# Optimization experiments

Hardware: AMD Instinct MI355X
Metric: run time of the kernel (lower is better)

## Reference

```python
import jax, jax.numpy as jnp
import numpy as np

NH = 32      # num_attention_heads
HD = 128     # head dim (kv_channels)
NG = 2       # multi_query_group_num
LAYER_NUMBER = 1


def apply_rotary_pos_emb(x, rope_cache):
    # x: [b, np, sq, hn]; rope_cache: [1, sq_max, rot/2, 2]
    b, nh, sq, hn = x.shape
    rot_dim = rope_cache.shape[-2] * 2
    xr, x_pass = x[..., :rot_dim], x[..., rot_dim:]
    xs = xr.reshape(b, nh, sq, rot_dim // 2, 2)
    c = rope_cache[:, :sq].reshape(-1, 1, sq, rot_dim // 2, 2)
    out = jnp.stack(
        [xs[..., 0] * c[..., 0] - xs[..., 1] * c[..., 1],
         xs[..., 1] * c[..., 0] + xs[..., 0] * c[..., 1]], axis=-1)
    out = out.reshape(b, nh, sq, rot_dim)
    return jnp.concatenate([out, x_pass], axis=-1)


def setup_inputs() -> dict:
    key = jax.random.key(0)
    ks = jax.random.split(key, 5)
    b, sq, h = 2, 2048, 4096
    qkv_out = NH * HD + 2 * NG * HD  # 4608
    return {
        "hidden_states": jax.random.normal(ks[0], (b, sq, h), jnp.float32),
        "rope_cache": jax.random.normal(ks[1], (1, sq, HD // 4, 2), jnp.float32),
        "W_qkv": jax.random.normal(ks[2], (h, qkv_out), jnp.float32) * 0.02,
        "b_qkv": jax.random.normal(ks[3], (qkv_out,), jnp.float32) * 0.02,
        "W_dense": jax.random.normal(ks[4], (NH * HD, h), jnp.float32) * 0.02,
    }


def reference(hidden_states, rope_cache, W_qkv, b_qkv, W_dense):
    b, sq, h = hidden_states.shape
    mixed = hidden_states @ W_qkv + b_qkv  # [b, sq, nh*hd + 2*ng*hd]
    q_sz = NH * HD
    kv_sz = NG * HD
    q = mixed[..., :q_sz].reshape(b, sq, NH, HD).transpose(0, 2, 1, 3)          # [b,nh,sq,hd]
    k = mixed[..., q_sz:q_sz + kv_sz].reshape(b, sq, NG, HD).transpose(0, 2, 1, 3)  # [b,ng,sq,hd]
    v = mixed[..., q_sz + kv_sz:].reshape(b, sq, NG, HD).transpose(0, 2, 1, 3)      # [b,ng,sq,hd]

    q = apply_rotary_pos_emb(q, rope_cache)
    k = apply_rotary_pos_emb(k, rope_cache)

    # expand KV groups to full heads (multi-query attention)
    rep = NH // NG
    k = jnp.broadcast_to(k[:, :, None], (b, NG, rep, sq, HD)).reshape(b, NH, sq, HD)
    v = jnp.broadcast_to(v[:, :, None], (b, NG, rep, sq, HD)).reshape(b, NH, sq, HD)

    # CoreAttention (eager path, fp32 softmax, causal)
    coeff = float(max(1, LAYER_NUMBER))  # apply_query_key_layer_scaling
    norm_factor = np.sqrt(HD) * coeff
    scores = jnp.einsum("bhqd,bhkd->bhqk", q, k) / norm_factor
    scores = scores.astype(jnp.float32) * coeff
    causal = jnp.tril(jnp.ones((sq, sq), dtype=bool))
    scores = jnp.where(causal[None, None], scores, -jnp.inf)
    probs = jax.nn.softmax(scores, axis=-1).astype(v.dtype)
    context = jnp.einsum("bhqk,bhkd->bhqd", probs, v)   # [b,nh,sq,hd]
    context = context.transpose(0, 2, 1, 3).reshape(b, sq, NH * HD)
    return context @ W_dense
```

## Files before the change

### kernel.cpp

```cpp
#include <hip/hip_runtime.h>
#include <hip/hip_bf16.h>
#include <stdint.h>

#define B_    2
#define SQ    2048
#define H_    4096
#define NHEAD 32
#define HDIM  128
#define NGRP  2
#define QKVN  4608
#define SCALE 0.08838834764831845f
#define QSCALE (0.08838834764831845f * 1.4426950408889634f)

typedef __attribute__((ext_vector_type(8))) short bf16x8;
typedef __attribute__((ext_vector_type(4))) short bf16x4;
typedef __attribute__((ext_vector_type(4))) float f32x4;

__device__ __forceinline__ float b2f(short s) {
  union { float f; unsigned u; } x; x.u = ((unsigned)(unsigned short)s) << 16; return x.f;
}
__device__ __forceinline__ short f2b(float f) {
  union { float f; unsigned u; } x; x.f = f;
  unsigned r = x.u + 0x7fffu + ((x.u >> 16) & 1u);
  return (short)(r >> 16);
}
__device__ __forceinline__ void gll16(const void* g, void* l) {
  __builtin_amdgcn_global_load_lds(
      (const __attribute__((address_space(1))) unsigned int*)g,
      (__attribute__((address_space(3))) unsigned int*)l, 16, 0, 0);
}

__global__ void conv_f32_bf16(const float* __restrict__ x, short* __restrict__ y, int n) {
  int i = (blockIdx.x * blockDim.x + threadIdx.x) * 4;
  if (i >= n) return;
  float4 v = *(const float4*)(x + i);
  union { short s[4]; uint2 u; } o;
  o.s[0] = f2b(v.x); o.s[1] = f2b(v.y); o.s[2] = f2b(v.z); o.s[3] = f2b(v.w);
  *(uint2*)(y + i) = o.u;
}

__global__ void transpose_f32_bf16(const float* __restrict__ W, short* __restrict__ Wt,
                                   int R, int C) {
  __shared__ float tile[64][65];
  int c0 = blockIdx.x * 64, r0 = blockIdx.y * 64;
  int tx = threadIdx.x & 15, ty = threadIdx.x >> 4;
  #pragma unroll
  for (int i = 0; i < 4; ++i) {
    float4 v = *(const float4*)(W + (size_t)(r0 + ty + 16 * i) * C + c0 + tx * 4);
    tile[ty + 16 * i][tx * 4 + 0] = v.x;
    tile[ty + 16 * i][tx * 4 + 1] = v.y;
    tile[ty + 16 * i][tx * 4 + 2] = v.z;
    tile[ty + 16 * i][tx * 4 + 3] = v.w;
  }
  __syncthreads();
  #pragma unroll
  for (int i = 0; i < 4; ++i) {
    int orow = ty + 16 * i;
    bf16x4 o;
    #pragma unroll
    for (int j = 0; j < 4; ++j) o[j] = f2b(tile[tx * 4 + j][orow]);
    *(bf16x4*)(Wt + (size_t)(c0 + orow) * R + r0 + tx * 4) = o;
  }
}

template<bool BIAS, bool OUTF32>
__global__ __launch_bounds__(256, 2) void gemm_bf16(
    const short* __restrict__ A, const short* __restrict__ Bt,
    const float* __restrict__ bias, short* __restrict__ outb,
    float* __restrict__ outf, int M, int N, int K)
{
  __shared__ short smA[128 * 64];
  __shared__ short smB[128 * 64];
  const int t = threadIdx.x;
  const int l = t & 63;
  const int w = t >> 6;
  const int wr = w >> 1, wc = w & 1;
  const int m0 = blockIdx.y * 128, n0 = blockIdx.x * 128;

  const f32x4 z = {0.f, 0.f, 0.f, 0.f};
  f32x4 acc[4][4];
  #pragma unroll
  for (int m = 0; m < 4; ++m)
    #pragma unroll
    for (int n = 0; n < 4; ++n) acc[m][n] = z;

  for (int k0 = 0; k0 < K; k0 += 64) {
    __syncthreads();
    #pragma unroll
    for (int i = 0; i < 4; ++i) {
      int c = t + i * 256;
      int row = c >> 3, slot = c & 7;
      int ss = slot ^ (row & 7);
      gll16(A  + (size_t)(m0 + row) * K + k0 + ss * 8,
            (char*)smA + (i * 256 + w * 64) * 16);
      gll16(Bt + (size_t)(n0 + row) * K + k0 + ss * 8,
            (char*)smB + (i * 256 + w * 64) * 16);
    }
    __syncthreads();
    #pragma unroll
    for (int kk = 0; kk < 2; ++kk) {
      bf16x8 a[4], b[4];
      #pragma unroll
      for (int m = 0; m < 4; ++m) {
        int row = wr * 64 + m * 16 + (l & 15);
        int off = (kk * 64 + ((l >> 4) << 4)) ^ ((row & 7) << 4);
        a[m] = *(const bf16x8*)((const char*)smA + row * 128 + off);
      }
      #pragma unroll
      for (int n = 0; n < 4; ++n) {
        int row = wc * 64 + n * 16 + (l & 15);
        int off = (kk * 64 + ((l >> 4) << 4)) ^ ((row & 7) << 4);
        b[n] = *(const bf16x8*)((const char*)smB + row * 128 + off);
      }
      #pragma unroll
      for (int m = 0; m < 4; ++m)
        #pragma unroll
        for (int n = 0; n < 4; ++n)
          acc[m][n] = __builtin_amdgcn_mfma_f32_16x16x32_bf16(a[m], b[n], acc[m][n], 0, 0, 0);
    }
  }

  #pragma unroll
  for (int m = 0; m < 4; ++m) {
    int row = m0 + wr * 64 + m * 16 + ((l >> 4) << 2);
    #pragma unroll
    for (int n = 0; n < 4; ++n) {
      int col = n0 + wc * 64 + n * 16 + (l & 15);
      float bv = BIAS ? bias[col] : 0.f;
      #pragma unroll
      for (int j = 0; j < 4; ++j) {
        float vv = acc[m][n][j] + bv;
        if (OUTF32) outf[(size_t)(row + j) * N + col] = vv;
        else        outb[(size_t)(row + j) * N + col] = f2b(vv);
      }
    }
  }
}

__global__ void rope_split(const short* __restrict__ mixed, const float* __restrict__ rope,
                           short* __restrict__ qo, short* __restrict__ ko, short* __restrict__ vo)
{
  const int CH = QKVN / 8;
  int idx = blockIdx.x * blockDim.x + threadIdx.x;
  if (idx >= B_ * SQ * CH) return;
  int row = idx / CH;
  int cc = (idx - row * CH) * 8;
  int b = row >> 11, s = row & 2047;

  bf16x8 xv = *(const bf16x8*)(mixed + (size_t)row * QKVN + cc);
  float x[8];
  #pragma unroll
  for (int i = 0; i < 8; ++i) x[i] = b2f(xv[i]);

  int sect, hh, d = cc & 127;
  if (cc < 4096)      { sect = 0; hh = cc >> 7; }
  else if (cc < 4352) { sect = 1; hh = (cc - 4096) >> 7; }
  else                { sect = 2; hh = (cc - 4352) >> 7; }

  if (sect < 2 && d < 64) {
    float4 ca = *(const float4*)(rope + s * 64 + d);
    float4 cb = *(const float4*)(rope + s * 64 + d + 4);
    float t0;
    t0 = x[0]*ca.x - x[1]*ca.y; x[1] = x[1]*ca.x + x[0]*ca.y; x[0] = t0;
    t0 = x[2]*ca.z - x[3]*ca.w; x[3] = x[3]*ca.z + x[2]*ca.w; x[2] = t0;
    t0 = x[4]*cb.x - x[5]*cb.y; x[5] = x[5]*cb.x + x[4]*cb.y; x[4] = t0;
    t0 = x[6]*cb.z - x[7]*cb.w; x[7] = x[7]*cb.z + x[6]*cb.w; x[6] = t0;
  }
  if (sect == 0) {
    #pragma unroll
    for (int i = 0; i < 8; ++i) x[i] *= QSCALE;
  }

  short* dst; size_t oidx;
  if (sect == 0)      { dst = qo; oidx = (((size_t)(b * NHEAD + hh) * SQ) + s) * HDIM + d; }
  else if (sect == 1) { dst = ko; oidx = (((size_t)(b * NGRP + hh) * SQ) + s) * HDIM + d; }
  else                { dst = vo; oidx = (((size_t)(b * NGRP + hh) * SQ) + s) * HDIM + d; }
  bf16x8 ov;
  #pragma unroll
  for (int i = 0; i < 8; ++i) ov[i] = f2b(x[i]);
  *(bf16x8*)(dst + oidx) = ov;
}

__global__ __launch_bounds__(512, 2) void attn_fwd(
    const short* __restrict__ q, const short* __restrict__ k,
    const short* __restrict__ v, short* __restrict__ ctx)
{
  __shared__ short smem[8192 + 9216];
  short* smK = smem;
  short* smV = smem + 8192;

  const int h = blockIdx.y, b = blockIdx.z;
  const int g = h >> 4;
  const int t = threadIdx.x, l = t & 63, w = t >> 6;
  const int lq = l & 15, hi = l >> 4;

  const short* qbase = q + ((size_t)(b * NHEAD + h) * SQ) * HDIM;
  const short* kbase = k + ((size_t)(b * NGRP + g) * SQ) * HDIM;
  const short* vbase = v + ((size_t)(b * NGRP + g) * SQ) * HDIM;

  const f32x4 z = {0.f, 0.f, 0.f, 0.f};

  for (int pass = 0; pass < 2; ++pass) {
    const int s = pass ? (7 - (int)blockIdx.x) : (int)blockIdx.x;
    const int q0 = s * 256;
    const int qw = q0 + w * 32;
    const int nkt = 4 * s + 4;

    bf16x8 qf[2][4];
    #pragma unroll
    for (int fq = 0; fq < 2; ++fq)
      #pragma unroll
      for (int kf = 0; kf < 4; ++kf)
        qf[fq][kf] = *(const bf16x8*)(qbase + (size_t)(qw + fq * 16 + lq) * HDIM + kf * 32 + hi * 8);

    f32x4 of[2][8];
    #pragma unroll
    for (int a = 0; a < 2; ++a)
      #pragma unroll
      for (int d = 0; d < 8; ++d) of[a][d] = z;
    float mrow[2] = {-1e30f, -1e30f};
    float lrow[2] = {0.f, 0.f};

    for (int kt = 0; kt < nkt; ++kt) {
      const int kb = kt * 64;
      __syncthreads();
      #pragma unroll
      for (int i = 0; i < 2; ++i) {
        int c = t + i * 512;
        int row = c >> 4, slot = c & 15;
        int ss = slot ^ (row & 7);
        gll16(kbase + (size_t)(kb + row) * HDIM + ss * 8,
              (char*)smK + (i * 512 + w * 64) * 16);
      }
      #pragma unroll
      for (int i = 0; i < 2; ++i) {
        int c = t + i * 512;
        int key = c & 63, d0 = (c >> 6) << 3;
        bf16x8 vv = *(const bf16x8*)(vbase + (size_t)(kb + key) * HDIM + d0);
        #pragma unroll
        for (int jj = 0; jj < 8; ++jj)
          smV[(d0 + jj) * 72 + key] = vv[jj];
      }
      __syncthreads();

      if (kb > qw + 31) continue;

      f32x4 st[2][4];
      #pragma unroll
      for (int fq = 0; fq < 2; ++fq)
        #pragma unroll
        for (int fk = 0; fk < 4; ++fk) st[fq][fk] = z;
      __builtin_amdgcn_s_setprio(1);
      #pragma unroll
      for (int kf = 0; kf < 4; ++kf) {
        bf16x8 kfr[4];
        #pragma unroll
        for (int fk = 0; fk < 4; ++fk) {
          int row = fk * 16 + lq;
          int slot = (kf * 4 + hi) ^ (row & 7);
          kfr[fk] = *(const bf16x8*)((const char*)smK + row * 256 + slot * 16);
        }
        #pragma unroll
        for (int fq = 0; fq < 2; ++fq)
          #pragma unroll
          for (int fk = 0; fk < 4; ++fk)
            st[fq][fk] = __builtin_amdgcn_mfma_f32_16x16x32_bf16(kfr[fk], qf[fq][kf], st[fq][fk], 0, 0, 0);
      }
      __builtin_amdgcn_s_setprio(0);

      bf16x4 pa[2][4];
      #pragma unroll
      for (int fq = 0; fq < 2; ++fq) {
        float sv[16];
        #pragma unroll
        for (int fk = 0; fk < 4; ++fk)
          #pragma unroll
          for (int j = 0; j < 4; ++j) sv[fk * 4 + j] = st[fq][fk][j];
        if (kb + 63 > qw + fq * 16) {
          int qrow = qw + fq * 16 + lq;
          #pragma unroll
          for (int fk = 0; fk < 4; ++fk)
            #pragma unroll
            for (int j = 0; j < 4; ++j)
              if (kb + fk * 16 + hi * 4 + j > qrow) sv[fk * 4 + j] = -1e30f;
        }
        float mx = sv[0];
        #pragma unroll
        for (int i = 1; i < 16; ++i) mx = fmaxf(mx, sv[i]);
        mx = fmaxf(mx, __shfl_xor(mx, 16));
        mx = fmaxf(mx, __shfl_xor(mx, 32));
        if (__any(mx > mrow[fq] + 11.0f)) {
          float mn = fmaxf(mrow[fq], mx);
          float corr = exp2f(mrow[fq] - mn);
          mrow[fq] = mn;
          lrow[fq] *= corr;
          float cj[4];
          #pragma unroll
          for (int j = 0; j < 4; ++j) cj[j] = __shfl(corr, hi * 4 + j);
          #pragma unroll
          for (int df = 0; df < 8; ++df)
            #pragma unroll
            for (int j = 0; j < 4; ++j) of[fq][df][j] *= cj[j];
        }
        float rs = 0.f;
        #pragma unroll
        for (int i = 0; i < 16; ++i) { sv[i] = exp2f(sv[i] - mrow[fq]); rs += sv[i]; }
        rs += __shfl_xor(rs, 16);
        rs += __shfl_xor(rs, 32);
        lrow[fq] += rs;
        #pragma unroll
        for (int fk = 0; fk < 4; ++fk) {
          bf16x4 p;
          p[0] = f2b(sv[fk * 4 + 0]); p[1] = f2b(sv[fk * 4 + 1]);
          p[2] = f2b(sv[fk * 4 + 2]); p[3] = f2b(sv[fk * 4 + 3]);
          pa[fq][fk] = p;
        }
      }

      __builtin_amdgcn_s_setprio(1);
      #pragma unroll
      for (int fk = 0; fk < 4; ++fk) {
        bf16x4 vb[8];
        #pragma unroll
        for (int df = 0; df < 8; ++df)
          vb[df] = *(const bf16x4*)(smV + (df * 16 + lq) * 72 + fk * 16 + hi * 4);
        #pragma unroll
        for (int df = 0; df < 8; ++df) {
          of[0][df] = __builtin_amdgcn_mfma_f32_16x16x16bf16_1k(pa[0][fk], vb[df], of[0][df], 0, 0, 0);
          of[1][df] = __builtin_amdgcn_mfma_f32_16x16x16bf16_1k(pa[1][fk], vb[df], of[1][df], 0, 0, 0);
        }
      }
      __builtin_amdgcn_s_setprio(0);
    }

    #pragma unroll
    for (int fq = 0; fq < 2; ++fq) {
      float inv = 1.f / lrow[fq];
      float ij[4];
      #pragma unroll
      for (int j = 0; j < 4; ++j) ij[j] = __shfl(inv, hi * 4 + j);
      #pragma unroll
      for (int j = 0; j < 4; ++j) {
        int srow = qw + fq * 16 + hi * 4 + j;
        size_t rbase = ((size_t)(b * SQ + srow)) * (NHEAD * HDIM) + (size_t)h * HDIM;
        #pragma unroll
        for (int df = 0; df < 8; ++df)
          ctx[rbase + df * 16 + lq] = f2b(of[fq][df][j] * ij[j]);
      }
    }
    __syncthreads();
  }
}

extern "C" void kernel_launch(void* const* d_in, const int* in_sizes, int n_in,
                              void* d_out, int out_size, void* d_ws, size_t ws_size,
                              hipStream_t stream)
{
  const float* hidden = (const float*)d_in[0];
  const float* rope   = (const float*)d_in[1];
  const float* Wqkv   = (const float*)d_in[2];
  const float* bqkv   = (const float*)d_in[3];
  const float* Wd     = (const float*)d_in[4];
  float* out = (float*)d_out;

  if (ws_size < 113246208ULL) return;
  char* ws = (char*)d_ws;
  short* hsb   = (short*)(ws);
  short* wT    = (short*)(ws + 33554432);
  short* mixed = (short*)(ws + 71303168);
  short* k_r   = (short*)(ws + 109051904);
  short* v_r   = (short*)(ws + 111149056);

  conv_f32_bf16<<<16384, 256, 0, stream>>>(hidden, hsb, B_ * SQ * H_);
  transpose_f32_bf16<<<dim3(QKVN / 64, H_ / 64), 256, 0, stream>>>(Wqkv, wT, H_, QKVN);
  gemm_bf16<true, false><<<dim3(QKVN / 128, (B_ * SQ) / 128), 256, 0, stream>>>(
      hsb, wT, bqkv, mixed, nullptr, B_ * SQ, QKVN, H_);
  rope_split<<<9216, 256, 0, stream>>>(mixed, rope, hsb, k_r, v_r);
  transpose_f32_bf16<<<dim3(H_ / 64, H_ / 64), 256, 0, stream>>>(Wd, wT, H_, H_);
  attn_fwd<<<dim3(4, NHEAD, B_), 512, 0, stream>>>(hsb, k_r, v_r, mixed);
  gemm_bf16<false, true><<<dim3(H_ / 128, (B_ * SQ) / 128), 256, 0, stream>>>(
      mixed, wT, nullptr, nullptr, out, B_ * SQ, H_, H_);
}
```

Measured before the change: 538.6 us.

## Replace dense output GEMM with 256x256-tile, 8-wave phased pipelined kernel

Swaps the final context@W_dense GEMM from the generic 128x128 bf16 kernel to a new kernel with 256x256 tiles, 512 threads and 128KB of double-buffered shared memory. Direct global-to-LDS loads use an XOR swizzle and are spread across four compute phases per K step. MFMA sections run at raised wave priority to overlap loads with math. The larger tile cuts global traffic per FLOP, but the grid shrinks to 256 blocks and the kernel uses heavy LDS and registers, which limits occupancy.

```diff
diff --git a/kernel.cpp b/kernel.cpp
--- a/kernel.cpp
+++ b/kernel.cpp
@@ -133,6 +133,110 @@
         if (OUTF32) outf[(size_t)(row + j) * N + col] = vv;
         else        outb[(size_t)(row + j) * N + col] = f2b(vv);
       }
+    }
+  }
+}
+
+__global__ __launch_bounds__(512, 2) void gemm8ph(
+    const short* __restrict__ A, const short* __restrict__ Bt,
+    float* __restrict__ outf, int M, int N, int K, int nbx)
+{
+  __shared__ char sm[131072];
+  const int t = threadIdx.x, l = t & 63, w = t >> 6;
+  const int lq = l & 15, hi = l >> 4;
+  const int wm = w >> 2, wn = w & 3;
+  const int by = (int)blockIdx.x / nbx, bx = (int)blockIdx.x % nbx;
+  const int m0 = by * 256, n0 = bx * 256;
+  const int nkt = K >> 6;
+
+  auto stage = [&](int tt, int s) {
+    if (tt >= nkt) return;
+    int kb = tt << 6;
+    const short* base = (s < 2) ? Bt + (size_t)(n0 + (s << 7)) * K
+                                : A  + (size_t)(m0 + ((s - 2) << 7)) * K;
+    char* dst = sm + ((tt & 1) << 16) + (s < 2 ? 32768 + (s << 14) : ((s - 2) << 14));
+    #pragma unroll
+    for (int i = 0; i < 2; ++i) {
+      int c = (i << 9) + t;
+      int row = c >> 3, sl = c & 7;
+      gll16(base + (size_t)row * K + kb + ((sl ^ (row & 7)) << 3), dst + c * 16);
+    }
+  };
+
+  const f32x4 z = {0.f, 0.f, 0.f, 0.f};
+  f32x4 acc[8][4];
+  #pragma unroll
+  for (int i = 0; i < 8; ++i)
+    #pragma unroll
+    for (int j = 0; j < 4; ++j) acc[i][j] = z;
+
+  bf16x8 aC[2][2], bC[4][2];
+
+  stage(0, 0); stage(0, 1); stage(0, 2); stage(0, 3);
+  stage(1, 0); stage(1, 1); stage(1, 2);
+  asm volatile("s_waitcnt vmcnt(6)" ::: "memory");
+  __builtin_amdgcn_s_barrier();
+
+#define PH(P, STT, STS, TAILV)                                              \
+  {                                                                         \
+    if ((P) == 0) {                                                         \
+      _Pragma("unroll")                                                     \
+      for (int fn = 0; fn < 4; ++fn) {                                      \
+        int rb = (wn << 6) + (fn << 4) + lq;                                \
+        const char* bb = sm + (bsel << 16) + 32768 + ((rb >> 7) << 14)      \
+                         + (rb & 127) * 128;                                \
+        _Pragma("unroll")                                                   \
+        for (int kk = 0; kk < 2; ++kk)                                      \
+          bC[fn][kk] = *(const bf16x8*)(bb + ((((kk << 2) + hi) ^ (rb & 7)) << 4)); \
+      }                                                                     \
+    }                                                                       \
+    _Pragma("unroll")                                                       \
+    for (int fr = 0; fr < 2; ++fr) {                                        \
+      int lr = ((P) << 5) + (fr << 4) + lq;                                 \
+      const char* ab = sm + (bsel << 16) + (wm << 14) + lr * 128;           \
+      _Pragma("unroll")                                                     \
+      for (int kk = 0; kk < 2; ++kk)                                        \
+        aC[fr][kk] = *(const bf16x8*)(ab + ((((kk << 2) + hi) ^ (lr & 7)) << 4)); \
+    }                                                                       \
+    stage((STT), (STS));                                                    \
+    __builtin_amdgcn_s_barrier();                                           \
+    asm volatile("s_waitcnt lgkmcnt(0)" ::: "memory");                      \
+    __builtin_amdgcn_s_setprio(1);                                          \
+    _Pragma("unroll")                                                       \
+    for (int kk = 0; kk < 2; ++kk)                                          \
+      _Pragma("unroll")                                                     \
+      for (int fr = 0; fr < 2; ++fr)                                        \
+        _Pragma("unroll")                                                   \
+        for (int fn = 0; fn < 4; ++fn)                                      \
+          acc[(P) * 2 + fr][fn] = __builtin_amdgcn_mfma_f32_16x16x32_bf16(  \
+              aC[fr][kk], bC[fn][kk], acc[(P) * 2 + fr][fn], 0, 0, 0);      \
+    __builtin_amdgcn_s_setprio(0);                                          \
+    if ((P) == 3) {                                                         \
+      if (TAILV) asm volatile("s_waitcnt vmcnt(0)" ::: "memory");           \
+      else       asm volatile("s_waitcnt vmcnt(6)" ::: "memory");           \
+    }                                                                       \
+    __builtin_amdgcn_s_barrier();                                           \
+  }
+
+  for (int T = 0; T < nkt; ++T) {
+    const int bsel = T & 1;
+    const bool tail = (T >= nkt - 2);
+    PH(0, T + 1, 3, tail)
+    PH(1, T + 2, 0, tail)
+    PH(2, T + 2, 1, tail)
+    PH(3, T + 2, 2, tail)
+  }
+#undef PH
+
+  #pragma unroll
+  for (int fm = 0; fm < 8; ++fm) {
+    int r0 = m0 + (wm << 7) + (fm << 4) + (hi << 2);
+    #pragma unroll
+    for (int fn = 0; fn < 4; ++fn) {
+      int cc = n0 + (wn << 6) + (fn << 4) + lq;
+      #pragma unroll
+      for (int j = 0; j < 4; ++j)
+        outf[(size_t)(r0 + j) * N + cc] = acc[fm][fn][j];
     }
   }
 }
@@ -378,6 +482,5 @@
   rope_split<<<9216, 256, 0, stream>>>(mixed, rope, hsb, k_r, v_r);
   transpose_f32_bf16<<<dim3(H_ / 64, H_ / 64), 256, 0, stream>>>(Wd, wT, H_, H_);
   attn_fwd<<<dim3(4, NHEAD, B_), 512, 0, stream>>>(hsb, k_r, v_r, mixed);
-  gemm_bf16<false, true><<<dim3(H_ / 128, (B_ * SQ) / 128), 256, 0, stream>>>(
-      mixed, wT, nullptr, nullptr, out, B_ * SQ, H_, H_);
-}
+  gemm8ph<<<256, 512, 0, stream>>>(mixed, wT, out, B_ * SQ, H_, H_, H_ / 256);
+}
```

Result: slower. 552.4 us (+2.6%).

## Double-buffer K/V tiles in attention kernel to overlap loads with compute

Applied to the files above, without the earlier changes.

Splits the shared-memory K and V tiles into two buffers and issues the global loads for the next key tile before computing the current one. The V transpose store into LDS is deferred until after the MFMA work, and there is now one barrier per iteration instead of two. This is meant to hide global-memory latency behind the QK and PV matrix math. In exchange, LDS use doubles (about 69KB per block), which may limit the two-blocks-per-CU occupancy, and the prefetched V values stay live in registers across the compute.

```diff
diff --git a/kernel.cpp b/kernel.cpp
--- a/kernel.cpp
+++ b/kernel.cpp
@@ -185,9 +185,7 @@
     const short* __restrict__ q, const short* __restrict__ k,
     const short* __restrict__ v, short* __restrict__ ctx)
 {
-  __shared__ short smem[8192 + 9216];
-  short* smK = smem;
-  short* smV = smem + 8192;
+  __shared__ short smem[2 * (8192 + 9216)];
 
   const int h = blockIdx.y, b = blockIdx.z;
   const int g = h >> 4;
@@ -197,6 +195,12 @@
   const short* qbase = q + ((size_t)(b * NHEAD + h) * SQ) * HDIM;
   const short* kbase = k + ((size_t)(b * NGRP + g) * SQ) * HDIM;
   const short* vbase = v + ((size_t)(b * NGRP + g) * SQ) * HDIM;
+
+  const int kc0 = t, kc1 = t + 512;
+  const int krow0 = kc0 >> 4, kss0 = (kc0 & 15) ^ (krow0 & 7);
+  const int krow1 = kc1 >> 4, kss1 = (kc1 & 15) ^ (krow1 & 7);
+  const int vkey0 = kc0 & 63, vd0 = (kc0 >> 6) << 3;
+  const int vkey1 = kc1 & 63, vd1 = (kc1 >> 6) << 3;
 
   const f32x4 z = {0.f, 0.f, 0.f, 0.f};
 
@@ -221,116 +225,135 @@
     float mrow[2] = {-1e30f, -1e30f};
     float lrow[2] = {0.f, 0.f};
 
+    {
+      short* K0 = smem;
+      short* V0 = smem + 16384;
+      gll16(kbase + (size_t)krow0 * HDIM + kss0 * 8, (char*)K0 + kc0 * 16);
+      gll16(kbase + (size_t)krow1 * HDIM + kss1 * 8, (char*)K0 + kc1 * 16);
+      bf16x8 vv0 = *(const bf16x8*)(vbase + (size_t)vkey0 * HDIM + vd0);
+      bf16x8 vv1 = *(const bf16x8*)(vbase + (size_t)vkey1 * HDIM + vd1);
+      #pragma unroll
+      for (int jj = 0; jj < 8; ++jj) V0[(vd0 + jj) * 72 + vkey0] = vv0[jj];
+      #pragma unroll
+      for (int jj = 0; jj < 8; ++jj) V0[(vd1 + jj) * 72 + vkey1] = vv1[jj];
+    }
+    __syncthreads();
+
     for (int kt = 0; kt < nkt; ++kt) {
       const int kb = kt * 64;
-      __syncthreads();
-      #pragma unroll
-      for (int i = 0; i < 2; ++i) {
-        int c = t + i * 512;
-        int row = c >> 4, slot = c & 15;
-        int ss = slot ^ (row & 7);
-        gll16(kbase + (size_t)(kb + row) * HDIM + ss * 8,
-              (char*)smK + (i * 512 + w * 64) * 16);
-      }
-      #pragma unroll
-      for (int i = 0; i < 2; ++i) {
-        int c = t + i * 512;
-        int key = c & 63, d0 = (c >> 6) << 3;
-        bf16x8 vv = *(const bf16x8*)(vbase + (size_t)(kb + key) * HDIM + d0);
-        #pragma unroll
-        for (int jj = 0; jj < 8; ++jj)
-          smV[(d0 + jj) * 72 + key] = vv[jj];
-      }
-      __syncthreads();
-
-      if (kb > qw + 31) continue;
-
-      f32x4 st[2][4];
-      #pragma unroll
-      for (int fq = 0; fq < 2; ++fq)
-        #pragma unroll
-        for (int fk = 0; fk < 4; ++fk) st[fq][fk] = z;
-      __builtin_amdgcn_s_setprio(1);
-      #pragma unroll
-      for (int kf = 0; kf < 4; ++kf) {
-        bf16x8 kfr[4];
-        #pragma unroll
-        for (int fk = 0; fk < 4; ++fk) {
-          int row = fk * 16 + lq;
-          int slot = (kf * 4 + hi) ^ (row & 7);
-          kfr[fk] = *(const bf16x8*)((const char*)smK + row * 256 + slot * 16);
+      const int cur = kt & 1;
+      const short* Kc = smem + cur * 8192;
+      const short* Vc = smem + 16384 + cur * 9216;
+      short* Kn = smem + (cur ^ 1) * 8192;
+      short* Vn = smem + 16384 + (cur ^ 1) * 9216;
+      const bool have_next = (kt + 1 < nkt);
+
+      bf16x8 vv0, vv1;
+      if (have_next) {
+        const int kbn = kb + 64;
+        gll16(kbase + (size_t)(kbn + krow0) * HDIM + kss0 * 8, (char*)Kn + kc0 * 16);
+        gll16(kbase + (size_t)(kbn + krow1) * HDIM + kss1 * 8, (char*)Kn + kc1 * 16);
+        vv0 = *(const bf16x8*)(vbase + (size_t)(kbn + vkey0) * HDIM + vd0);
+        vv1 = *(const bf16x8*)(vbase + (size_t)(kbn + vkey1) * HDIM + vd1);
+        __builtin_amdgcn_sched_barrier(0);
+      }
+
+      if (kb <= qw + 31) {
+        f32x4 st[2][4];
+        #pragma unroll
+        for (int fq = 0; fq < 2; ++fq)
+          #pragma unroll
+          for (int fk = 0; fk < 4; ++fk) st[fq][fk] = z;
+        __builtin_amdgcn_s_setprio(1);
+        #pragma unroll
+        for (int kf = 0; kf < 4; ++kf) {
+          bf16x8 kfr[4];
+          #pragma unroll
+          for (int fk = 0; fk < 4; ++fk) {
+            int row = fk * 16 + lq;
+            int slot = (kf * 4 + hi) ^ (row & 7);
+            kfr[fk] = *(const bf16x8*)((const char*)Kc + row * 256 + slot * 16);
+          }
+          #pragma unroll
+          for (int fq = 0; fq < 2; ++fq)
+            #pragma unroll
+            for (int fk = 0; fk < 4; ++fk)
+              st[fq][fk] = __builtin_amdgcn_mfma_f32_16x16x32_bf16(kfr[fk], qf[fq][kf], st[fq][fk], 0, 0, 0);
         }
-        #pragma unroll
-        for (int fq = 0; fq < 2; ++fq)
-          #pragma unroll
-          for (int fk = 0; fk < 4; ++fk)
-            st[fq][fk] = __builtin_amdgcn_mfma_f32_16x16x32_bf16(kfr[fk], qf[fq][kf], st[fq][fk], 0, 0, 0);
-      }
-      __builtin_amdgcn_s_setprio(0);
-
-      bf16x4 pa[2][4];
-      #pragma unroll
-      for (int fq = 0; fq < 2; ++fq) {
-        float sv[16];
-        #pragma unroll
-        for (int fk = 0; fk < 4; ++fk)
-          #pragma unroll
-          for (int j = 0; j < 4; ++j) sv[fk * 4 + j] = st[fq][fk][j];
-        if (kb + 63 > qw + fq * 16) {
-          int qrow = qw + fq * 16 + lq;
+        __builtin_amdgcn_s_setprio(0);
+
+        bf16x4 pa[2][4];
+        #pragma unroll
+        for (int fq = 0; fq < 2; ++fq) {
+          float sv[16];
           #pragma unroll
           for (int fk = 0; fk < 4; ++fk)
             #pragma unroll
-            for (int j = 0; j < 4; ++j)
-              if (kb + fk * 16 + hi * 4 + j > qrow) sv[fk * 4 + j] = -1e30f;
+            for (int j = 0; j < 4; ++j) sv[fk * 4 + j] = st[fq][fk][j];
+          if (kb + 63 > qw + fq * 16) {
+            int qrow = qw + fq * 16 + lq;
+            #pragma unroll
+            for (int fk = 0; fk < 4; ++fk)
+              #pragma unroll
+              for (int j = 0; j < 4; ++j)
+                if (kb + fk * 16 + hi * 4 + j > qrow) sv[fk * 4 + j] = -1e30f;
+          }
+          float mx = sv[0];
+          #pragma unroll
+          for (int i = 1; i < 16; ++i) mx = fmaxf(mx, sv[i]);
+          mx = fmaxf(mx, __shfl_xor(mx, 16));
+          mx = fmaxf(mx, __shfl_xor(mx, 32));
+          if (__any(mx > mrow[fq] + 11.0f)) {
+            float mn = fmaxf(mrow[fq], mx);
+            float corr = exp2f(mrow[fq] - mn);
+            mrow[fq] = mn;
+            lrow[fq] *= corr;
+            float cj[4];
+            #pragma unroll
+            for (int j = 0; j < 4; ++j) cj[j] = __shfl(corr, hi * 4 + j);
+            #pragma unroll
+            for (int df = 0; df < 8; ++df)
+              #pragma unroll
+              for (int j = 0; j < 4; ++j) of[fq][df][j] *= cj[j];
+          }
+          float rs = 0.f;
+          #pragma unroll
+          for (int i = 0; i < 16; ++i) { sv[i] = exp2f(sv[i] - mrow[fq]); rs += sv[i]; }
+          rs += __shfl_xor(rs, 16);
+          rs += __shfl_xor(rs, 32);
+          lrow[fq] += rs;
+          #pragma unroll
+          for (int fk = 0; fk < 4; ++fk) {
+            bf16x4 p;
+            p[0] = f2b(sv[fk * 4 + 0]); p[1] = f2b(sv[fk * 4 + 1]);
+            p[2] = f2b(sv[fk * 4 + 2]); p[3] = f2b(sv[fk * 4 + 3]);
+            pa[fq][fk] = p;
+          }
         }
-        float mx = sv[0];
-        #pragma unroll
-        for (int i = 1; i < 16; ++i) mx = fmaxf(mx, sv[i]);
-        mx = fmaxf(mx, __shfl_xor(mx, 16));
-        mx = fmaxf(mx, __shfl_xor(mx, 32));
-        if (__any(mx > mrow[fq] + 11.0f)) {
-          float mn = fmaxf(mrow[fq], mx);
-          float corr = exp2f(mrow[fq] - mn);
-          mrow[fq] = mn;
-          lrow[fq] *= corr;
-          float cj[4];
-          #pragma unroll
-          for (int j = 0; j < 4; ++j) cj[j] = __shfl(corr, hi * 4 + j);
+
+        __builtin_amdgcn_s_setprio(1);
+        #pragma unroll
+        for (int fk = 0; fk < 4; ++fk) {
+          bf16x4 vb[8];
           #pragma unroll
           for (int df = 0; df < 8; ++df)
-            #pragma unroll
-            for (int j = 0; j < 4; ++j) of[fq][df][j] *= cj[j];
+            vb[df] = *(const bf16x4*)(Vc + (df * 16 + lq) * 72 + fk * 16 + hi * 4);
+          #pragma unroll
+          for (int df = 0; df < 8; ++df) {
+            of[0][df] = __builtin_amdgcn_mfma_f32_16x16x16bf16_1k(pa[0][fk], vb[df], of[0][df], 0, 0, 0);
+            of[1][df] = __builtin_amdgcn_mfma_f32_16x16x16bf16_1k(pa[1][fk], vb[df], of[1][df], 0, 0, 0);
+          }
         }
-        float rs = 0.f;
-        #pragma unroll
-        for (int i = 0; i < 16; ++i) { sv[i] = exp2f(sv[i] - mrow[fq]); rs += sv[i]; }
-        rs += __shfl_xor(rs, 16);
-        rs += __shfl_xor(rs, 32);
-        lrow[fq] += rs;
-        #pragma unroll
-        for (int fk = 0; fk < 4; ++fk) {
-          bf16x4 p;
-          p[0] = f2b(sv[fk * 4 + 0]); p[1] = f2b(sv[fk * 4 + 1]);
-          p[2] = f2b(sv[fk * 4 + 2]); p[3] = f2b(sv[fk * 4 + 3]);
-          pa[fq][fk] = p;
-        }
-      }
-
-      __builtin_amdgcn_s_setprio(1);
-      #pragma unroll
-      for (int fk = 0; fk < 4; ++fk) {
-        bf16x4 vb[8];
-        #pragma unroll
-        for (int df = 0; df < 8; ++df)
-          vb[df] = *(const bf16x4*)(smV + (df * 16 + lq) * 72 + fk * 16 + hi * 4);
-        #pragma unroll
-        for (int df = 0; df < 8; ++df) {
-          of[0][df] = __builtin_amdgcn_mfma_f32_16x16x16bf16_1k(pa[0][fk], vb[df], of[0][df], 0, 0, 0);
-          of[1][df] = __builtin_amdgcn_mfma_f32_16x16x16bf16_1k(pa[1][fk], vb[df], of[1][df], 0, 0, 0);
-        }
-      }
-      __builtin_amdgcn_s_setprio(0);
+        __builtin_amdgcn_s_setprio(0);
+      }
+
+      if (have_next) {
+        #pragma unroll
+        for (int jj = 0; jj < 8; ++jj) Vn[(vd0 + jj) * 72 + vkey0] = vv0[jj];
+        #pragma unroll
+        for (int jj = 0; jj < 8; ++jj) Vn[(vd1 + jj) * 72 + vkey1] = vv1[jj];
+      }
+      __syncthreads();
     }
 
     #pragma unroll
```

Result: no change. 529.3 us (-1.7%).
